# Optimization experiments

Hardware: AMD Instinct MI355X
Metric: run time of the kernel (lower is better)

## Reference

```python
import jax, jax.numpy as jnp
import numpy as np

LS = (0, 1, 2)
M_IN = (128, 64, 32)            # input mults per l -> dim 480
M_MID = (384, 192, 96)          # gated mlp_mid mults; scalars=384, gated l=1,2
N_GATES = M_MID[1] + M_MID[2]   # 288 extra 0e gate scalars
M1_OUT = (M_MID[0] + N_GATES, M_MID[1], M_MID[2])  # fctp_1 output mults (672,192,96)
M_OUT = (128, 64, 32)           # output mults -> dim 480


def _split(x, mults):
    """Split flat (N, sum mul*(2l+1)) features into per-l (N, mul, 2l+1) blocks."""
    outs, off = [], 0
    for m, l in zip(mults, LS):
        d = m * (2 * l + 1)
        outs.append(x[:, off:off + d].reshape(x.shape[0], m, 2 * l + 1))
        off += d
    return outs


def _fctp(xs, attr, Ws, b):
    """FCTP with a 1x0e second operand: per-l linear mix * attr, 1/sqrt(fan_in)
    path normalization, bias on the l=0 block (Equiformer rescale convention)."""
    outs = []
    for x, W in zip(xs, Ws):
        inv = 1.0 / np.sqrt(x.shape[1]).astype(np.float32)
        y = jnp.einsum('nmi,mo->noi', x, W) * inv * attr[:, :, None]
        outs.append(y)
    outs[0] = outs[0] + b[None, :, None]
    return outs


def _ffn(node_input, node_attr, W1_0, W1_1, W1_2, b1, W2_0, W2_1, W2_2, b2):
    xs = _split(node_input, M_IN)
    h = _fctp(xs, node_attr, (W1_0, W1_1, W1_2), b1)
    # SwishGate: silu on scalars, sigmoid gates multiply the l>0 irreps
    s0 = h[0][:, :, 0]                         # (N, 672)
    scalars = jax.nn.silu(s0[:, :M_MID[0]])    # (N, 384)
    gates = jax.nn.sigmoid(s0[:, M_MID[0]:])   # (N, 288)
    g1 = gates[:, :M_MID[1]]
    g2 = gates[:, M_MID[1]:]
    mid = [scalars[:, :, None], h[1] * g1[:, :, None], h[2] * g2[:, :, None]]
    out = _fctp(mid, node_attr, (W2_0, W2_1, W2_2), b2)
    return jnp.concatenate([o.reshape(o.shape[0], -1) for o in out], axis=1)


def setup_inputs() -> dict:
    key = jax.random.key(0)
    ks = jax.random.split(key, 9)
    N = 100000
    return {
        'node_input': jax.random.normal(ks[0], (N, 480), jnp.float32),
        'node_attr': jnp.ones((N, 1), jnp.float32),
        'W1_0': jax.random.normal(ks[1], (128, 672), jnp.float32),
        'W1_1': jax.random.normal(ks[2], (64, 192), jnp.float32),
        'W1_2': jax.random.normal(ks[3], (32, 96), jnp.float32),
        'b1': jax.random.normal(ks[4], (672,), jnp.float32),
        'W2_0': jax.random.normal(ks[5], (384, 128), jnp.float32),
        'W2_1': jax.random.normal(ks[6], (192, 64), jnp.float32),
        'W2_2': jax.random.normal(ks[7], (96, 32), jnp.float32),
        'b2': jax.random.normal(ks[8], (128,), jnp.float32),
    }


def reference(node_input, node_attr, W1_0, W1_1, W1_2, b1, W2_0, W2_1, W2_2, b2):
    return _ffn(node_input, node_attr, W1_0, W1_1, W1_2, b1, W2_0, W2_1, W2_2, b2)
```

## Files before the change

kernel.cpp:

```cpp
#include <hip/hip_runtime.h>
#include <hip/hip_bf16.h>

typedef __bf16 bf16_t;
typedef __bf16 bf16x8 __attribute__((ext_vector_type(8)));
typedef float  f32x4  __attribute__((ext_vector_type(4)));

static __device__ __forceinline__ f32x4 mfma16(bf16x8 a, bf16x8 b, f32x4 c) {
    return __builtin_amdgcn_mfma_f32_16x16x32_bf16(a, b, c, 0, 0, 0);
}
static __device__ __forceinline__ float fast_rcp(float x) {
    return __builtin_amdgcn_rcpf(x);
}

#define OFF_W10 0
#define OFF_W11 86016
#define OFF_W12 98304
#define OFF_W20 101376
#define OFF_W21 150528
#define OFF_W22 162816
#define W_TOTAL 165888

__global__ void prep_weights(const float* __restrict__ W10, const float* __restrict__ W11,
                             const float* __restrict__ W12, const float* __restrict__ W20,
                             const float* __restrict__ W21, const float* __restrict__ W22,
                             bf16_t* __restrict__ ws) {
    int idx = blockIdx.x * 256 + threadIdx.x;
    if (idx >= W_TOTAL) return;
    const float* src; int K, N, off;
    if      (idx < OFF_W11) { src = W10; K = 128; N = 672; off = OFF_W10; }
    else if (idx < OFF_W12) { src = W11; K = 64;  N = 192; off = OFF_W11; }
    else if (idx < OFF_W20) { src = W12; K = 32;  N = 96;  off = OFF_W12; }
    else if (idx < OFF_W21) { src = W20; K = 384; N = 128; off = OFF_W20; }
    else if (idx < OFF_W22) { src = W21; K = 192; N = 64;  off = OFF_W21; }
    else                    { src = W22; K = 96;  N = 32;  off = OFF_W22; }
    int local = idx - off;
    int j    = local & 7;
    int lane = (local >> 3) & 63;
    int tf   = local >> 9;
    int frags = K >> 5;
    int f    = tf % frags;
    int tile = tf / frags;
    int k = f * 32 + ((lane >> 4) << 3) + j;
    int n = tile * 16 + (lane & 15);
    ws[idx] = (bf16_t)src[k * N + n];
}

#define XDE_S   488
#define MID0_S  392
#define MID1_S  200
#define MID2_S  104
#define GATE_S  296
#define MID0_B  9600
#define MID2_B  9600

__global__ __launch_bounds__(256, 3)
void ffn_kernel(const float* __restrict__ x, const float* __restrict__ attr,
                const float* __restrict__ b1, const float* __restrict__ b2,
                const bf16_t* __restrict__ wf, float* __restrict__ out) {
    __shared__ bf16_t smid[17920];
    __shared__ bf16_t sgate[16 * GATE_S];
    __shared__ float  sattr[16];
    __shared__ float  sb1[672];
    __shared__ float  sb2[128];

    const int tid   = threadIdx.x;
    const int lane  = tid & 63;
    const int w     = tid >> 6;
    const int rlane = lane & 15;
    const int q     = lane >> 4;
    const int rowbase = blockIdx.x * 16;

    for (int it = 0; it < 8; ++it) {
        int idx = tid + it * 256;
        if (idx < 1920) {
            int row = idx / 120;
            int c4  = idx - row * 120;
            const float4 v = ((const float4*)(x + (size_t)(rowbase + row) * 480))[c4];
            float vals[4] = {v.x, v.y, v.z, v.w};
            int base = c4 * 4;
#pragma unroll
            for (int e = 0; e < 4; ++e) {
                int col = base + e;
                int dc;
                if (col < 128) dc = col;
                else if (col < 320) { int r = col - 128; int m = r / 3; int i = r - m * 3; dc = 128 + i * 64 + m; }
                else                { int r = col - 320; int m = r / 5; int i = r - m * 5; dc = 320 + i * 32 + m; }
                smid[row * XDE_S + dc] = (bf16_t)vals[e];
            }
        }
    }
    for (int i = tid; i < 672; i += 256) sb1[i] = b1[i];
    if (tid < 128) sb2[tid] = b2[tid];
    if (tid < 16)  sattr[tid] = attr[rowbase + tid];
    __syncthreads();

    float sat[4];
#pragma unroll
    for (int r = 0; r < 4; ++r) sat[r] = sattr[q * 4 + r];

    bf16x8 a0[4], a1[3][2], a2[5];
    {
        int rb = rlane * XDE_S + q * 8;
#pragma unroll
        for (int f = 0; f < 4; ++f) a0[f] = *(const bf16x8*)&smid[rb + f * 32];
#pragma unroll
        for (int i = 0; i < 3; ++i)
#pragma unroll
            for (int f = 0; f < 2; ++f) a1[i][f] = *(const bf16x8*)&smid[rb + 128 + i * 64 + f * 32];
#pragma unroll
        for (int i = 0; i < 5; ++i) a2[i] = *(const bf16x8*)&smid[rb + 320 + i * 32];
    }

    {
        const float inv = 0.088388347648318447f;
        const bf16_t* base10 = wf + OFF_W10 + (lane << 3);
        int t = w;
        bf16x8 bc[4];
        {
            const bf16_t* p = base10 + ((t * 4) << 9);
#pragma unroll
            for (int f = 0; f < 4; ++f) bc[f] = *(const bf16x8*)(p + (f << 9));
        }
        while (t < 42) {
            int tn = t + 4;
            bf16x8 bn[4] = {bc[0], bc[1], bc[2], bc[3]};
            if (tn < 42) {
                const bf16_t* p = base10 + ((tn * 4) << 9);
#pragma unroll
                for (int f = 0; f < 4; ++f) bn[f] = *(const bf16x8*)(p + (f << 9));
            }
            f32x4 acc = {0.f, 0.f, 0.f, 0.f};
#pragma unroll
            for (int f = 0; f < 4; ++f) acc = mfma16(a0[f], bc[f], acc);

            int c = t * 16 + rlane;
            float bias = sb1[c];
            if (t < 24) {
#pragma unroll
                for (int r = 0; r < 4; ++r) {
                    float v = acc[r] * inv * sat[r] + bias;
                    float s = v * fast_rcp(1.f + __expf(-v));
                    smid[MID0_B + (q * 4 + r) * MID0_S + c] = (bf16_t)s;
                }
            } else {
#pragma unroll
                for (int r = 0; r < 4; ++r) {
                    float v = acc[r] * inv * sat[r] + bias;
                    float g = fast_rcp(1.f + __expf(-v));
                    sgate[(q * 4 + r) * GATE_S + (c - 384)] = (bf16_t)g;
                }
            }
#pragma unroll
            for (int f = 0; f < 4; ++f) bc[f] = bn[f];
            t = tn;
        }
    }
    __syncthreads();

    {
        const float inv = 0.051031036307982884f;
        bf16x8 am[12];
        int rb = MID0_B + rlane * MID0_S + q * 8;
#pragma unroll
        for (int f = 0; f < 12; ++f) am[f] = *(const bf16x8*)&smid[rb + f * 32];
#pragma unroll 2
        for (int t = w; t < 8; t += 4) {
            const bf16_t* p = wf + OFF_W20 + ((t * 12) << 9) + (lane << 3);
            f32x4 acc = {0.f, 0.f, 0.f, 0.f};
#pragma unroll
            for (int f = 0; f < 12; ++f) {
                bf16x8 b = *(const bf16x8*)(p + (f << 9));
                acc = mfma16(am[f], b, acc);
            }
            int c = t * 16 + rlane;
            float bias = sb2[c];
#pragma unroll
            for (int r = 0; r < 4; ++r)
                out[(size_t)(rowbase + q * 4 + r) * 480 + c] = acc[r] * inv * sat[r] + bias;
        }
    }
    {
        const float inv = 0.125f;
#pragma unroll 3
        for (int t = w; t < 12; t += 4) {
            const bf16_t* p = wf + OFF_W11 + ((t * 2) << 9) + (lane << 3);
            bf16x8 b0 = *(const bf16x8*)p;
            bf16x8 b1f = *(const bf16x8*)(p + 512);
            f32x4 acc[3];
#pragma unroll
            for (int i = 0; i < 3; ++i) {
                f32x4 a = {0.f, 0.f, 0.f, 0.f};
                a = mfma16(a1[i][0], b0, a);
                a = mfma16(a1[i][1], b1f, a);
                acc[i] = a;
            }
            int m = t * 16 + rlane;
#pragma unroll
            for (int r = 0; r < 4; ++r) {
                int row = q * 4 + r;
                float g = (float)sgate[row * GATE_S + m] * inv * sat[r];
#pragma unroll
                for (int i = 0; i < 3; ++i)
                    smid[i * 3200 + row * MID1_S + m] = (bf16_t)(acc[i][r] * g);
            }
        }
    }
    __syncthreads();

    {
        const float inv = 0.17677669529663689f;
#pragma unroll 2
        for (int t = w; t < 6; t += 4) {
            const bf16_t* p = wf + OFF_W12 + (t << 9) + (lane << 3);
            bf16x8 b = *(const bf16x8*)p;
            f32x4 acc[5];
#pragma unroll
            for (int i = 0; i < 5; ++i) {
                f32x4 a = {0.f, 0.f, 0.f, 0.f};
                acc[i] = mfma16(a2[i], b, a);
            }
            int m = t * 16 + rlane;
#pragma unroll
            for (int r = 0; r < 4; ++r) {
                int row = q * 4 + r;
                float g = (float)sgate[row * GATE_S + 192 + m] * inv * sat[r];
#pragma unroll
                for (int i = 0; i < 5; ++i)
                    smid[MID2_B + i * 1664 + row * MID2_S + m] = (bf16_t)(acc[i][r] * g);
            }
        }
    }
    {
        const float inv = 0.072168783648703220f;
        int t = w;
        const bf16_t* p = wf + OFF_W21 + ((t * 6) << 9) + (lane << 3);
        bf16x8 b[6];
#pragma unroll
        for (int f = 0; f < 6; ++f) b[f] = *(const bf16x8*)(p + (f << 9));
        f32x4 acc[3];
#pragma unroll
        for (int i = 0; i < 3; ++i) {
            bf16x8 am[6];
            int rb = i * 3200 + rlane * MID1_S + q * 8;
#pragma unroll
            for (int f = 0; f < 6; ++f) am[f] = *(const bf16x8*)&smid[rb + f * 32];
            f32x4 a = {0.f, 0.f, 0.f, 0.f};
#pragma unroll
            for (int f = 0; f < 6; ++f) a = mfma16(am[f], b[f], a);
            acc[i] = a;
        }
        int o = t * 16 + rlane;
#pragma unroll
        for (int r = 0; r < 4; ++r) {
            float s = inv * sat[r];
            float* dst = out + (size_t)(rowbase + q * 4 + r) * 480 + 128 + o * 3;
            dst[0] = acc[0][r] * s;
            dst[1] = acc[1][r] * s;
            dst[2] = acc[2][r] * s;
        }
    }
    __syncthreads();

    if (w < 2) {
        const float inv = 0.10206207261596575f;
        int t = w;
        const bf16_t* p = wf + OFF_W22 + ((t * 3) << 9) + (lane << 3);
        bf16x8 b[3];
#pragma unroll
        for (int f = 0; f < 3; ++f) b[f] = *(const bf16x8*)(p + (f << 9));
        f32x4 acc[5];
#pragma unroll
        for (int i = 0; i < 5; ++i) {
            bf16x8 am[3];
            int rb = MID2_B + i * 1664 + rlane * MID2_S + q * 8;
#pragma unroll
            for (int f = 0; f < 3; ++f) am[f] = *(const bf16x8*)&smid[rb + f * 32];
            f32x4 a = {0.f, 0.f, 0.f, 0.f};
#pragma unroll
            for (int f = 0; f < 3; ++f) a = mfma16(am[f], b[f], a);
            acc[i] = a;
        }
        int o = t * 16 + rlane;
#pragma unroll
        for (int r = 0; r < 4; ++r) {
            float s = inv * sat[r];
            float* dst = out + (size_t)(rowbase + q * 4 + r) * 480 + 320 + o * 5;
#pragma unroll
            for (int i = 0; i < 5; ++i) dst[i] = acc[i][r] * s;
        }
    }
}

extern "C" void kernel_launch(void* const* d_in, const int* in_sizes, int n_in,
                              void* d_out, int out_size, void* d_ws, size_t ws_size,
                              hipStream_t stream) {
    const float* x    = (const float*)d_in[0];
    const float* attr = (const float*)d_in[1];
    const float* W10  = (const float*)d_in[2];
    const float* W11  = (const float*)d_in[3];
    const float* W12  = (const float*)d_in[4];
    const float* b1   = (const float*)d_in[5];
    const float* W20  = (const float*)d_in[6];
    const float* W21  = (const float*)d_in[7];
    const float* W22  = (const float*)d_in[8];
    const float* b2   = (const float*)d_in[9];
    float*  out = (float*)d_out;
    bf16_t* wf  = (bf16_t*)d_ws;

    int N = in_sizes[0] / 480;

    prep_weights<<<dim3((W_TOTAL + 255) / 256), dim3(256), 0, stream>>>(
        W10, W11, W12, W20, W21, W22, wf);
    ffn_kernel<<<dim3(N / 16), dim3(256), 0, stream>>>(
        x, attr, b1, b2, wf, out);
}
```

Measured before the change: 449.0 us.

## Keep gates in registers, drop bias/gate LDS, raise occupancy, add MFMA priority

Gate sigmoid values are kept in per-thread registers instead of a shared-memory gate buffer, because the tiles that compute them map to the same wave and lane that later consume them. Biases are read directly from global memory rather than staged in LDS, and the launch bound moves to 4 blocks per SM. Together these cut LDS usage so more blocks can be resident. The software-prefetch double buffer for W1_0 is removed, s_setprio raises wave priority around the MFMA chains, and the weight prep kernel now reads its source coalesced and scatters on write. The extra registers held for gate values and the loss of prefetching could cause spills or stalls under the tighter register budget.

```diff
diff --git a/kernel.cpp b/kernel.cpp
--- a/kernel.cpp
+++ b/kernel.cpp
@@ -20,48 +20,45 @@
 #define OFF_W22 162816
 #define W_TOTAL 165888
 
+template<int K, int N, int OFF>
+static __device__ __forceinline__ void scatter_seg(const float* __restrict__ src,
+                                                   bf16_t* __restrict__ ws, int local) {
+    int k  = local / N;
+    int n  = local - k * N;
+    int f  = k >> 5;
+    int kr = k & 31;
+    int lane = ((kr >> 3) << 4) | (n & 15);
+    int dst  = OFF + ((((n >> 4) * (K >> 5)) + f) << 9) + (lane << 3) + (kr & 7);
+    ws[dst] = (bf16_t)src[local];
+}
+
 __global__ void prep_weights(const float* __restrict__ W10, const float* __restrict__ W11,
                              const float* __restrict__ W12, const float* __restrict__ W20,
                              const float* __restrict__ W21, const float* __restrict__ W22,
                              bf16_t* __restrict__ ws) {
     int idx = blockIdx.x * 256 + threadIdx.x;
     if (idx >= W_TOTAL) return;
-    const float* src; int K, N, off;
-    if      (idx < OFF_W11) { src = W10; K = 128; N = 672; off = OFF_W10; }
-    else if (idx < OFF_W12) { src = W11; K = 64;  N = 192; off = OFF_W11; }
-    else if (idx < OFF_W20) { src = W12; K = 32;  N = 96;  off = OFF_W12; }
-    else if (idx < OFF_W21) { src = W20; K = 384; N = 128; off = OFF_W20; }
-    else if (idx < OFF_W22) { src = W21; K = 192; N = 64;  off = OFF_W21; }
-    else                    { src = W22; K = 96;  N = 32;  off = OFF_W22; }
-    int local = idx - off;
-    int j    = local & 7;
-    int lane = (local >> 3) & 63;
-    int tf   = local >> 9;
-    int frags = K >> 5;
-    int f    = tf % frags;
-    int tile = tf / frags;
-    int k = f * 32 + ((lane >> 4) << 3) + j;
-    int n = tile * 16 + (lane & 15);
-    ws[idx] = (bf16_t)src[k * N + n];
+    if      (idx < OFF_W11) scatter_seg<128, 672, OFF_W10>(W10, ws, idx - OFF_W10);
+    else if (idx < OFF_W12) scatter_seg< 64, 192, OFF_W11>(W11, ws, idx - OFF_W11);
+    else if (idx < OFF_W20) scatter_seg< 32,  96, OFF_W12>(W12, ws, idx - OFF_W12);
+    else if (idx < OFF_W21) scatter_seg<384, 128, OFF_W20>(W20, ws, idx - OFF_W20);
+    else if (idx < OFF_W22) scatter_seg<192,  64, OFF_W21>(W21, ws, idx - OFF_W21);
+    else                    scatter_seg< 96,  32, OFF_W22>(W22, ws, idx - OFF_W22);
 }
 
 #define XDE_S   488
 #define MID0_S  392
 #define MID1_S  200
 #define MID2_S  104
-#define GATE_S  296
 #define MID0_B  9600
 #define MID2_B  9600
 
-__global__ __launch_bounds__(256, 3)
+__global__ __launch_bounds__(256, 4)
 void ffn_kernel(const float* __restrict__ x, const float* __restrict__ attr,
                 const float* __restrict__ b1, const float* __restrict__ b2,
                 const bf16_t* __restrict__ wf, float* __restrict__ out) {
     __shared__ bf16_t smid[17920];
-    __shared__ bf16_t sgate[16 * GATE_S];
     __shared__ float  sattr[16];
-    __shared__ float  sb1[672];
-    __shared__ float  sb2[128];
 
     const int tid   = threadIdx.x;
     const int lane  = tid & 63;
@@ -89,9 +86,7 @@
             }
         }
     }
-    for (int i = tid; i < 672; i += 256) sb1[i] = b1[i];
-    if (tid < 128) sb2[tid] = b2[tid];
-    if (tid < 16)  sattr[tid] = attr[rowbase + tid];
+    if (tid < 16) sattr[tid] = attr[rowbase + tid];
     __syncthreads();
 
     float sat[4];
@@ -110,49 +105,46 @@
 #pragma unroll
         for (int i = 0; i < 5; ++i) a2[i] = *(const bf16x8*)&smid[rb + 320 + i * 32];
     }
+
+    float gv[5][4];
 
     {
         const float inv = 0.088388347648318447f;
         const bf16_t* base10 = wf + OFF_W10 + (lane << 3);
-        int t = w;
-        bf16x8 bc[4];
-        {
+#pragma unroll
+        for (int ti = 0; ti < 6; ++ti) {
+            int t = w + ti * 4;
             const bf16_t* p = base10 + ((t * 4) << 9);
-#pragma unroll
-            for (int f = 0; f < 4; ++f) bc[f] = *(const bf16x8*)(p + (f << 9));
-        }
-        while (t < 42) {
-            int tn = t + 4;
-            bf16x8 bn[4] = {bc[0], bc[1], bc[2], bc[3]};
-            if (tn < 42) {
-                const bf16_t* p = base10 + ((tn * 4) << 9);
-#pragma unroll
-                for (int f = 0; f < 4; ++f) bn[f] = *(const bf16x8*)(p + (f << 9));
-            }
+            float bias = b1[t * 16 + rlane];
             f32x4 acc = {0.f, 0.f, 0.f, 0.f};
-#pragma unroll
-            for (int f = 0; f < 4; ++f) acc = mfma16(a0[f], bc[f], acc);
-
+            __builtin_amdgcn_s_setprio(1);
+#pragma unroll
+            for (int f = 0; f < 4; ++f) acc = mfma16(a0[f], *(const bf16x8*)(p + (f << 9)), acc);
+            __builtin_amdgcn_s_setprio(0);
             int c = t * 16 + rlane;
-            float bias = sb1[c];
-            if (t < 24) {
-#pragma unroll
-                for (int r = 0; r < 4; ++r) {
-                    float v = acc[r] * inv * sat[r] + bias;
-                    float s = v * fast_rcp(1.f + __expf(-v));
-                    smid[MID0_B + (q * 4 + r) * MID0_S + c] = (bf16_t)s;
-                }
-            } else {
-#pragma unroll
-                for (int r = 0; r < 4; ++r) {
-                    float v = acc[r] * inv * sat[r] + bias;
-                    float g = fast_rcp(1.f + __expf(-v));
-                    sgate[(q * 4 + r) * GATE_S + (c - 384)] = (bf16_t)g;
-                }
-            }
-#pragma unroll
-            for (int f = 0; f < 4; ++f) bc[f] = bn[f];
-            t = tn;
+#pragma unroll
+            for (int r = 0; r < 4; ++r) {
+                float v = acc[r] * inv * sat[r] + bias;
+                float s = v * fast_rcp(1.f + __expf(-v));
+                smid[MID0_B + (q * 4 + r) * MID0_S + c] = (bf16_t)s;
+            }
+        }
+#pragma unroll
+        for (int ti = 0; ti < 5; ++ti) {
+            int t = 24 + w + ti * 4;
+            if (ti == 4 && t >= 42) continue;
+            const bf16_t* p = base10 + ((t * 4) << 9);
+            float bias = b1[t * 16 + rlane];
+            f32x4 acc = {0.f, 0.f, 0.f, 0.f};
+            __builtin_amdgcn_s_setprio(1);
+#pragma unroll
+            for (int f = 0; f < 4; ++f) acc = mfma16(a0[f], *(const bf16x8*)(p + (f << 9)), acc);
+            __builtin_amdgcn_s_setprio(0);
+#pragma unroll
+            for (int r = 0; r < 4; ++r) {
+                float v = acc[r] * inv * sat[r] + bias;
+                gv[ti][r] = fast_rcp(1.f + __expf(-v));
+            }
         }
     }
     __syncthreads();
@@ -163,17 +155,17 @@
         int rb = MID0_B + rlane * MID0_S + q * 8;
 #pragma unroll
         for (int f = 0; f < 12; ++f) am[f] = *(const bf16x8*)&smid[rb + f * 32];
-#pragma unroll 2
-        for (int t = w; t < 8; t += 4) {
+#pragma unroll
+        for (int ti = 0; ti < 2; ++ti) {
+            int t = w + ti * 4;
             const bf16_t* p = wf + OFF_W20 + ((t * 12) << 9) + (lane << 3);
+            float bias = b2[t * 16 + rlane];
             f32x4 acc = {0.f, 0.f, 0.f, 0.f};
-#pragma unroll
-            for (int f = 0; f < 12; ++f) {
-                bf16x8 b = *(const bf16x8*)(p + (f << 9));
-                acc = mfma16(am[f], b, acc);
-            }
+            __builtin_amdgcn_s_setprio(1);
+#pragma unroll
+            for (int f = 0; f < 12; ++f) acc = mfma16(am[f], *(const bf16x8*)(p + (f << 9)), acc);
+            __builtin_amdgcn_s_setprio(0);
             int c = t * 16 + rlane;
-            float bias = sb2[c];
 #pragma unroll
             for (int r = 0; r < 4; ++r)
                 out[(size_t)(rowbase + q * 4 + r) * 480 + c] = acc[r] * inv * sat[r] + bias;
@@ -181,12 +173,14 @@
     }
     {
         const float inv = 0.125f;
-#pragma unroll 3
-        for (int t = w; t < 12; t += 4) {
+#pragma unroll
+        for (int ti = 0; ti < 3; ++ti) {
+            int t = w + ti * 4;
             const bf16_t* p = wf + OFF_W11 + ((t * 2) << 9) + (lane << 3);
-            bf16x8 b0 = *(const bf16x8*)p;
+            bf16x8 b0  = *(const bf16x8*)p;
             bf16x8 b1f = *(const bf16x8*)(p + 512);
             f32x4 acc[3];
+            __builtin_amdgcn_s_setprio(1);
 #pragma unroll
             for (int i = 0; i < 3; ++i) {
                 f32x4 a = {0.f, 0.f, 0.f, 0.f};
@@ -194,11 +188,12 @@
                 a = mfma16(a1[i][1], b1f, a);
                 acc[i] = a;
             }
+            __builtin_amdgcn_s_setprio(0);
             int m = t * 16 + rlane;
 #pragma unroll
             for (int r = 0; r < 4; ++r) {
                 int row = q * 4 + r;
-                float g = (float)sgate[row * GATE_S + m] * inv * sat[r];
+                float g = gv[ti][r] * inv * sat[r];
 #pragma unroll
                 for (int i = 0; i < 3; ++i)
                     smid[i * 3200 + row * MID1_S + m] = (bf16_t)(acc[i][r] * g);
@@ -209,21 +204,25 @@
 
     {
         const float inv = 0.17677669529663689f;
-#pragma unroll 2
-        for (int t = w; t < 6; t += 4) {
+#pragma unroll
+        for (int ti = 0; ti < 2; ++ti) {
+            int t = w + ti * 4;
+            if (ti == 1 && t >= 6) continue;
             const bf16_t* p = wf + OFF_W12 + (t << 9) + (lane << 3);
             bf16x8 b = *(const bf16x8*)p;
             f32x4 acc[5];
+            __builtin_amdgcn_s_setprio(1);
 #pragma unroll
             for (int i = 0; i < 5; ++i) {
                 f32x4 a = {0.f, 0.f, 0.f, 0.f};
                 acc[i] = mfma16(a2[i], b, a);
             }
+            __builtin_amdgcn_s_setprio(0);
             int m = t * 16 + rlane;
 #pragma unroll
             for (int r = 0; r < 4; ++r) {
                 int row = q * 4 + r;
-                float g = (float)sgate[row * GATE_S + 192 + m] * inv * sat[r];
+                float g = gv[3 + ti][r] * inv * sat[r];
 #pragma unroll
                 for (int i = 0; i < 5; ++i)
                     smid[MID2_B + i * 1664 + row * MID2_S + m] = (bf16_t)(acc[i][r] * g);
@@ -238,6 +237,7 @@
 #pragma unroll
         for (int f = 0; f < 6; ++f) b[f] = *(const bf16x8*)(p + (f << 9));
         f32x4 acc[3];
+        __builtin_amdgcn_s_setprio(1);
 #pragma unroll
         for (int i = 0; i < 3; ++i) {
             bf16x8 am[6];
@@ -249,6 +249,7 @@
             for (int f = 0; f < 6; ++f) a = mfma16(am[f], b[f], a);
             acc[i] = a;
         }
+        __builtin_amdgcn_s_setprio(0);
         int o = t * 16 + rlane;
 #pragma unroll
         for (int r = 0; r < 4; ++r) {
@@ -269,6 +270,7 @@
 #pragma unroll
         for (int f = 0; f < 3; ++f) b[f] = *(const bf16x8*)(p + (f << 9));
         f32x4 acc[5];
+        __builtin_amdgcn_s_setprio(1);
 #pragma unroll
         for (int i = 0; i < 5; ++i) {
             bf16x8 am[3];
@@ -280,6 +282,7 @@
             for (int f = 0; f < 3; ++f) a = mfma16(am[f], b[f], a);
             acc[i] = a;
         }
+        __builtin_amdgcn_s_setprio(0);
         int o = t * 16 + rlane;
 #pragma unroll
         for (int r = 0; r < 4; ++r) {
```

Result: slower. 483.8 us (+7.8%).
